# Performance work log

Measured on AMD Instinct MI355X. Metric: run time of the kernel, lower is better.

## Reference

```python
import jax, jax.numpy as jnp
import numpy as np

DIM = 1024
NUM_HEADS = 16
MASKED = True


def setup_inputs() -> dict:
    key = jax.random.key(0)
    ks = jax.random.split(key, 9)
    B, S, D = 2, 2048, DIM
    return {
        "x": jax.random.normal(ks[0], (B, S, D), dtype=jnp.float32),
        "Wq": jax.random.normal(ks[1], (D, D), dtype=jnp.float32),
        "bq": jax.random.normal(ks[2], (D,), dtype=jnp.float32),
        "Wk": jax.random.normal(ks[3], (D, D), dtype=jnp.float32),
        "bk": jax.random.normal(ks[4], (D,), dtype=jnp.float32),
        "Wv": jax.random.normal(ks[5], (D, D), dtype=jnp.float32),
        "bv": jax.random.normal(ks[6], (D,), dtype=jnp.float32),
        "Wo": jax.random.normal(ks[7], (D, D), dtype=jnp.float32),
        "bo": jax.random.normal(ks[8], (D,), dtype=jnp.float32),
    }


def _mha(x, Wq, bq, Wk, bk, Wv, bv, Wo, bo):
    B, S, D = x.shape
    H = NUM_HEADS
    hd = D // H
    # projections (torch Linear stores [out,in]; here W is [out,in], x @ W.T + b)
    q = x @ Wq.T + bq
    k = x @ Wk.T + bk
    v = x @ Wv.T + bv
    # [B, H, S, hd]
    q = q.reshape(B, S, H, hd).transpose(0, 2, 1, 3)
    k = k.reshape(B, S, H, hd).transpose(0, 2, 1, 3)
    v = v.reshape(B, S, H, hd).transpose(0, 2, 1, 3)
    scores = jnp.einsum("bhqd,bhkd->bhqk", q, k) / jnp.sqrt(jnp.asarray(hd, x.dtype))
    if MASKED:
        mask = jnp.tril(jnp.ones((S, S), dtype=bool))
        scores = jnp.where(mask, scores, -jnp.inf)
    attn = jax.nn.softmax(scores, axis=-1)
    out = jnp.einsum("bhqk,bhkd->bhqd", attn, v)
    out = out.transpose(0, 2, 1, 3).reshape(B, S, D)
    return out @ Wo.T + bo


def reference(x, Wq, bq, Wk, bk, Wv, bv, Wo, bo):
    return _mha(x, Wq, bq, Wk, bk, Wv, bv, Wo, bo)
```

## Files before the change

kernel.cpp:

```cpp
#include <hip/hip_runtime.h>

typedef unsigned short u16;
typedef unsigned int u32;
typedef __attribute__((ext_vector_type(4))) float f32x4;
typedef __attribute__((ext_vector_type(8))) __bf16 bf16x8;

#define L2E 1.4426950408889634f

__device__ __forceinline__ u16 f2bf(float f) { return __builtin_bit_cast(u16, (__bf16)f); }
__device__ __forceinline__ float bf2f(u16 h) { return (float)__builtin_bit_cast(__bf16, h); }
__device__ __forceinline__ f32x4 mfma16(bf16x8 a, bf16x8 b, f32x4 c) {
  return __builtin_amdgcn_mfma_f32_16x16x32_bf16(a, b, c, 0, 0, 0);
}
__device__ __forceinline__ void gl_lds16(const u16* g, u16* l) {
  __builtin_amdgcn_global_load_lds((__attribute__((address_space(1))) void*)g,
                                   (__attribute__((address_space(3))) void*)l,
                                   16, 0, 0);
}
__device__ __forceinline__ f32x4 fzero() {
  f32x4 v = {0.f, 0.f, 0.f, 0.f};
  return v;
}

__global__ void k_prep(const float* __restrict__ x, const float* __restrict__ Wq,
                       const float* __restrict__ Wk, const float* __restrict__ Wv,
                       const float* __restrict__ Wo,
                       u16* __restrict__ xh, u16* __restrict__ xl,
                       u16* __restrict__ wqh, u16* __restrict__ wql,
                       u16* __restrict__ wkh, u16* __restrict__ wkl,
                       u16* __restrict__ wvb, u16* __restrict__ wob) {
  int i = (blockIdx.x * 256 + threadIdx.x) * 4;
  const float* src;
  u16* hi;
  u16* lo;
  int j;
  if (i < 4194304)      { src = x;  hi = xh;  lo = xl;      j = i; }
  else if (i < 5242880) { src = Wq; hi = wqh; lo = wql;     j = i - 4194304; }
  else if (i < 6291456) { src = Wk; hi = wkh; lo = wkl;     j = i - 5242880; }
  else if (i < 7340032) { src = Wv; hi = wvb; lo = nullptr; j = i - 6291456; }
  else                  { src = Wo; hi = wob; lo = nullptr; j = i - 7340032; }
  float4 v = *(const float4*)(src + j);
  float vv[4] = {v.x, v.y, v.z, v.w};
  u16 hh[4];
#pragma unroll
  for (int t = 0; t < 4; ++t) hh[t] = f2bf(vv[t]);
  *(ushort4*)(hi + j) = make_ushort4(hh[0], hh[1], hh[2], hh[3]);
  if (lo) {
    u16 ll[4];
#pragma unroll
    for (int t = 0; t < 4; ++t) ll[t] = f2bf(vv[t] - bf2f(hh[t]));
    *(ushort4*)(lo + j) = make_ushort4(ll[0], ll[1], ll[2], ll[3]);
  }
}

template <int SPLIT, int EPI>
__device__ __forceinline__ void gemm_body(
    u16* sm, const u16* __restrict__ Ah, const u16* __restrict__ Al,
    const u16* __restrict__ Bh, const u16* __restrict__ Bl,
    const float* __restrict__ bias, float scale,
    u16* __restrict__ oH, u16* __restrict__ oL, float* __restrict__ oF,
    int m0, int n0) {
  u16* sAh = sm;
  u16* sBh = sm + 8192;
  u16* sAl = SPLIT ? (sm + 16384) : sm;
  u16* sBl = SPLIT ? (sm + 24576) : sm;

  const int tid = threadIdx.x;
  const int lane = tid & 63, w = tid >> 6;
  const int wm = w >> 1, wn = w & 1;
  const int fr = lane & 15, fg = lane >> 4;
  const int strow = tid >> 3;
  const int stcb = (tid & 7) * 16;

  f32x4 acc[4][4];
#pragma unroll
  for (int i = 0; i < 4; ++i)
#pragma unroll
    for (int j = 0; j < 4; ++j) acc[i][j] = fzero();

  for (int kk = 0; kk < 1024; kk += 64) {
    __syncthreads();
#pragma unroll
    for (int c = 0; c < 4; ++c) {
      int row = c * 32 + strow;
      int srcc = (stcb ^ (((row >> 2) & 1) << 5)) >> 1;
      int dstc = row * 64 + (stcb >> 1);
      gl_lds16(Ah + (size_t)(m0 + row) * 1024 + kk + srcc, sAh + dstc);
      gl_lds16(Bh + (size_t)(n0 + row) * 1024 + kk + srcc, sBh + dstc);
      if constexpr (SPLIT) {
        gl_lds16(Al + (size_t)(m0 + row) * 1024 + kk + srcc, sAl + dstc);
        gl_lds16(Bl + (size_t)(n0 + row) * 1024 + kk + srcc, sBl + dstc);
      }
    }
    __syncthreads();

#pragma unroll
    for (int kk2 = 0; kk2 < 2; ++kk2) {
      bf16x8 ah[4], bh[4], al[4], bl[4];
#pragma unroll
      for (int i = 0; i < 4; ++i) {
        int ra = wm * 64 + i * 16 + fr;
        int ca = (kk2 * 64 + fg * 16) ^ (((ra >> 2) & 1) << 5);
        ah[i] = *(const bf16x8*)(sAh + ra * 64 + (ca >> 1));
        if constexpr (SPLIT) al[i] = *(const bf16x8*)(sAl + ra * 64 + (ca >> 1));
        int rb = wn * 64 + i * 16 + fr;
        int cb = (kk2 * 64 + fg * 16) ^ (((rb >> 2) & 1) << 5);
        bh[i] = *(const bf16x8*)(sBh + rb * 64 + (cb >> 1));
        if constexpr (SPLIT) bl[i] = *(const bf16x8*)(sBl + rb * 64 + (cb >> 1));
      }
      __builtin_amdgcn_s_setprio(1);
#pragma unroll
      for (int i = 0; i < 4; ++i)
#pragma unroll
        for (int j = 0; j < 4; ++j) {
          acc[i][j] = mfma16(ah[i], bh[j], acc[i][j]);
          if constexpr (SPLIT) {
            acc[i][j] = mfma16(ah[i], bl[j], acc[i][j]);
            acc[i][j] = mfma16(al[i], bh[j], acc[i][j]);
          }
        }
      __builtin_amdgcn_s_setprio(0);
    }
  }

#pragma unroll
  for (int i = 0; i < 4; ++i)
#pragma unroll
    for (int j = 0; j < 4; ++j) {
      int cg = n0 + wn * 64 + j * 16 + fr;
      float bv = bias[cg];
      if constexpr (EPI == 1) {
        int rgb = m0 + wm * 64 + i * 16 + fg * 4;
        int b = rgb >> 11, s = rgb & 2047, hd2 = cg >> 6, dd = cg & 63;
        u16 hv[4];
#pragma unroll
        for (int r = 0; r < 4; ++r) hv[r] = f2bf((acc[i][j][r] + bv) * scale);
        *(ushort4*)(oH + ((size_t)((b * 16 + hd2) * 64 + dd)) * 2048 + s) =
            make_ushort4(hv[0], hv[1], hv[2], hv[3]);
      } else {
#pragma unroll
        for (int r = 0; r < 4; ++r) {
          int rg = m0 + wm * 64 + i * 16 + fg * 4 + r;
          float val = (acc[i][j][r] + bv) * scale;
          if constexpr (EPI == 0) {
            int b = rg >> 11, s = rg & 2047, hd2 = cg >> 6, dd = cg & 63;
            size_t off = ((size_t)((b * 16 + hd2) * 2048 + s)) * 64 + dd;
            u16 hv = f2bf(val);
            oH[off] = hv;
            oL[off] = f2bf(val - bf2f(hv));
          } else {
            oF[(size_t)rg * 1024 + cg] = val;
          }
        }
      }
    }
}

__global__ __launch_bounds__(256, 2) void k_qkv(
    const u16* __restrict__ xh, const u16* __restrict__ xl,
    const u16* __restrict__ wqh, const u16* __restrict__ wql,
    const u16* __restrict__ wkh, const u16* __restrict__ wkl,
    const u16* __restrict__ wvb,
    const float* __restrict__ bq, const float* __restrict__ bk,
    const float* __restrict__ bv,
    u16* __restrict__ qh, u16* __restrict__ ql,
    u16* __restrict__ kh, u16* __restrict__ kl, u16* __restrict__ vt) {
  __shared__ u16 sm[32768];
  const int d = blockIdx.x;
  const int xcd = d & 7, j = d >> 3;
  const int m0 = (xcd * 4 + (j & 3)) * 128;
  const int pn = j >> 2;
  const int proj = pn >> 3, n0 = (pn & 7) * 128;
  if (proj == 0)
    gemm_body<1, 0>(sm, xh, xl, wqh, wql, bq, 0.125f * L2E, qh, ql, nullptr, m0, n0);
  else if (proj == 1)
    gemm_body<1, 0>(sm, xh, xl, wkh, wkl, bk, 1.0f, kh, kl, nullptr, m0, n0);
  else
    gemm_body<0, 1>(sm, xh, nullptr, wvb, nullptr, bv, 1.0f, vt, nullptr, nullptr, m0, n0);
}

__global__ __launch_bounds__(256, 4) void k_oproj(
    const u16* __restrict__ A, const u16* __restrict__ B,
    const float* __restrict__ bias, float* __restrict__ out) {
  __shared__ u16 sm[12288];
  u16* sA = sm;
  u16* sB = sm + 4096;

  const int tid = threadIdx.x;
  const int lane = tid & 63, w = tid >> 6;
  const int fr = lane & 15, fg = lane >> 4;
  const int m0 = blockIdx.x * 64, n0 = blockIdx.y * 128;
  const int strow = tid >> 3;
  const int stcb = (tid & 7) * 16;

  f32x4 acc[4][2];
#pragma unroll
  for (int i = 0; i < 4; ++i)
#pragma unroll
    for (int jj = 0; jj < 2; ++jj) acc[i][jj] = fzero();

  for (int kk = 0; kk < 1024; kk += 64) {
    __syncthreads();
#pragma unroll
    for (int c = 0; c < 2; ++c) {
      int row = c * 32 + strow;
      int srcc = (stcb ^ (((row >> 2) & 1) << 5)) >> 1;
      gl_lds16(A + (size_t)(m0 + row) * 1024 + kk + srcc, sA + row * 64 + (stcb >> 1));
    }
#pragma unroll
    for (int c = 0; c < 4; ++c) {
      int row = c * 32 + strow;
      int srcc = (stcb ^ (((row >> 2) & 1) << 5)) >> 1;
      gl_lds16(B + (size_t)(n0 + row) * 1024 + kk + srcc, sB + row * 64 + (stcb >> 1));
    }
    __syncthreads();

#pragma unroll
    for (int kk2 = 0; kk2 < 2; ++kk2) {
      bf16x8 af[4], bf_[2];
#pragma unroll
      for (int i = 0; i < 4; ++i) {
        int ra = i * 16 + fr;
        int ca = (kk2 * 64 + fg * 16) ^ (((ra >> 2) & 1) << 5);
        af[i] = *(const bf16x8*)(sA + ra * 64 + (ca >> 1));
      }
#pragma unroll
      for (int jj = 0; jj < 2; ++jj) {
        int rb = w * 32 + jj * 16 + fr;
        int cb = (kk2 * 64 + fg * 16) ^ (((rb >> 2) & 1) << 5);
        bf_[jj] = *(const bf16x8*)(sB + rb * 64 + (cb >> 1));
      }
      __builtin_amdgcn_s_setprio(1);
#pragma unroll
      for (int i = 0; i < 4; ++i)
#pragma unroll
        for (int jj = 0; jj < 2; ++jj) acc[i][jj] = mfma16(af[i], bf_[jj], acc[i][jj]);
      __builtin_amdgcn_s_setprio(0);
    }
  }

#pragma unroll
  for (int i = 0; i < 4; ++i)
#pragma unroll
    for (int jj = 0; jj < 2; ++jj) {
      int cg = n0 + w * 32 + jj * 16 + fr;
      float bv = bias[cg];
#pragma unroll
      for (int r = 0; r < 4; ++r) {
        int rg = m0 + i * 16 + fg * 4 + r;
        out[(size_t)rg * 1024 + cg] = acc[i][jj][r] + bv;
      }
    }
}

__global__ __launch_bounds__(512, 2) void k_attn(
    const u16* __restrict__ Qh, const u16* __restrict__ Ql,
    const u16* __restrict__ Kh, const u16* __restrict__ Kl,
    const u16* __restrict__ Vt, u16* __restrict__ Oa) {
  __shared__ u16 sKh[3][4096], sKl[3][4096], sVt[3][4096];
  __shared__ u16 sP[8][1024];

  const int tid = threadIdx.x;
  const int lane = tid & 63, w = tid >> 6;
  const int fr = lane & 15, fg = lane >> 4;

  const int d = blockIdx.x;
  const int g = d >> 3;
  const int bh = (d & 7) * 4 + (g & 3);
  const int pr = g >> 2;

  const size_t base = (size_t)bh * 131072;
  const u16* Qh_p = Qh + base;
  const u16* Ql_p = Ql + base;
  const u16* Kh_p = Kh + base;
  const u16* Kl_p = Kl + base;
  const u16* Vt_p = Vt + base;
  const int bb = bh >> 4, hh = bh & 15;

  const int srow8 = tid >> 3, scb8 = tid & 7;

  auto STAGE = [&](int t, int c) {
    int cbs = scb8 ^ (srow8 & 7);
    gl_lds16(Kh_p + ((size_t)(t * 64 + srow8)) * 64 + cbs * 8, &sKh[c][srow8 * 64 + scb8 * 8]);
    gl_lds16(Kl_p + ((size_t)(t * 64 + srow8)) * 64 + cbs * 8, &sKl[c][srow8 * 64 + scb8 * 8]);
    gl_lds16(Vt_p + (size_t)srow8 * 2048 + t * 64 + cbs * 8, &sVt[c][srow8 * 64 + scb8 * 8]);
  };

  for (int half = 0; half < 2; ++half) {
    const int j = half ? (15 - pr) : pr;
    const int nt = 2 * (j + 1);
    const int qrow = j * 128 + w * 16 + fr;

    if (half) asm volatile("s_barrier" ::: "memory");
    int cur = 0;
    STAGE(0, 0);

    bf16x8 qhf[2], qlf[2];
#pragma unroll
    for (int ks = 0; ks < 2; ++ks) {
      qhf[ks] = *(const bf16x8*)(Qh_p + (size_t)qrow * 64 + ks * 32 + fg * 8);
      qlf[ks] = *(const bf16x8*)(Ql_p + (size_t)qrow * 64 + ks * 32 + fg * 8);
    }

    float mx = -1e30f, l = 0.f;
    f32x4 o[4];
#pragma unroll
    for (int f = 0; f < 4; ++f) o[f] = fzero();

    for (int t = 0; t < nt; ++t) {
      int nxt = cur + 1;
      if (nxt == 3) nxt = 0;
      if (t + 1 < nt) {
        STAGE(t + 1, nxt);
        asm volatile("s_waitcnt vmcnt(3)" ::: "memory");
      } else {
        asm volatile("s_waitcnt vmcnt(0)" ::: "memory");
      }
      asm volatile("s_barrier" ::: "memory");

      const u16* kbh = sKh[cur];
      const u16* kbl = sKl[cur];
      const u16* vbb = sVt[cur];

      f32x4 sc[4];
      __builtin_amdgcn_s_setprio(1);
#pragma unroll
      for (int f = 0; f < 4; ++f) {
        f32x4 a = fzero();
#pragma unroll
        for (int ks = 0; ks < 2; ++ks) {
          int row = f * 16 + fr;
          int cb = (fg + 4 * ks) ^ (fr & 7);
          bf16x8 khv = *(const bf16x8*)(kbh + row * 64 + cb * 8);
          bf16x8 klv = *(const bf16x8*)(kbl + row * 64 + cb * 8);
          a = mfma16(khv, qhf[ks], a);
          a = mfma16(khv, qlf[ks], a);
          a = mfma16(klv, qhf[ks], a);
        }
        sc[f] = a;
      }
      __builtin_amdgcn_s_setprio(0);

      if (t >= nt - 2) {
#pragma unroll
        for (int f = 0; f < 4; ++f)
#pragma unroll
          for (int r = 0; r < 4; ++r) {
            int kvg = t * 64 + f * 16 + fg * 4 + r;
            if (kvg > qrow) sc[f][r] = -1e30f;
          }
      }

      float pm = -1e30f;
#pragma unroll
      for (int f = 0; f < 4; ++f)
#pragma unroll
        for (int r = 0; r < 4; ++r) pm = fmaxf(pm, sc[f][r]);
      pm = fmaxf(pm, __shfl_xor(pm, 16, 64));
      pm = fmaxf(pm, __shfl_xor(pm, 32, 64));

      const bool resc = __any(pm > mx + 11.5f);
      float alp = 1.0f;
      if (resc) {
        float mn = fmaxf(mx, pm);
        alp = exp2f(mx - mn);
        mx = mn;
      }

      float ps = 0.f;
#pragma unroll
      for (int f = 0; f < 4; ++f) {
        float p0 = exp2f(sc[f][0] - mx);
        float p1 = exp2f(sc[f][1] - mx);
        float p2 = exp2f(sc[f][2] - mx);
        float p3 = exp2f(sc[f][3] - mx);
        ps += (p0 + p1) + (p2 + p3);
        uint2 pv;
        pv.x = (u32)f2bf(p0) | ((u32)f2bf(p1) << 16);
        pv.y = (u32)f2bf(p2) | ((u32)f2bf(p3) << 16);
        int e = (f * 16 + fg * 4) ^ ((fr & 7) << 3);
        *(uint2*)(&sP[w][fr * 64 + e]) = pv;
      }
      ps += __shfl_xor(ps, 16, 64);
      ps += __shfl_xor(ps, 32, 64);
      l = l * alp + ps;

      if (resc) {
        float alpb[4];
#pragma unroll
        for (int r = 0; r < 4; ++r) alpb[r] = __shfl(alp, fg * 4 + r, 64);
#pragma unroll
        for (int f = 0; f < 4; ++f)
#pragma unroll
          for (int r = 0; r < 4; ++r) o[f][r] *= alpb[r];
      }

      __builtin_amdgcn_s_setprio(1);
#pragma unroll
      for (int ks = 0; ks < 2; ++ks) {
        int e = (ks * 32 + fg * 8) ^ ((fr & 7) << 3);
        bf16x8 pa = *(const bf16x8*)(&sP[w][fr * 64 + e]);
#pragma unroll
        for (int f = 0; f < 4; ++f) {
          int row = f * 16 + fr;
          int cb = (fg + 4 * ks) ^ (fr & 7);
          bf16x8 vb = *(const bf16x8*)(vbb + row * 64 + cb * 8);
          o[f] = mfma16(pa, vb, o[f]);
        }
      }
      __builtin_amdgcn_s_setprio(0);

      cur = nxt;
    }

    float lb[4];
#pragma unroll
    for (int r = 0; r < 4; ++r) lb[r] = __shfl(l, fg * 4 + r, 64);
#pragma unroll
    for (int f = 0; f < 4; ++f)
#pragma unroll
      for (int r = 0; r < 4; ++r) {
        int qg = j * 128 + w * 16 + fg * 4 + r;
        float val = o[f][r] / lb[r];
        Oa[((size_t)(bb * 2048 + qg)) * 1024 + hh * 64 + f * 16 + fr] = f2bf(val);
      }
  }
}

extern "C" void kernel_launch(void* const* d_in, const int* in_sizes, int n_in,
                              void* d_out, int out_size, void* d_ws, size_t ws_size,
                              hipStream_t stream) {
  const float* x  = (const float*)d_in[0];
  const float* Wq = (const float*)d_in[1];
  const float* bq = (const float*)d_in[2];
  const float* Wk = (const float*)d_in[3];
  const float* bk = (const float*)d_in[4];
  const float* Wv = (const float*)d_in[5];
  const float* bv = (const float*)d_in[6];
  const float* Wo = (const float*)d_in[7];
  const float* bo = (const float*)d_in[8];
  float* out = (float*)d_out;

  u16* ws  = (u16*)d_ws;
  u16* xh  = ws;
  u16* xl  = xh + 4194304;
  u16* wqh = xl + 4194304;
  u16* wql = wqh + 1048576;
  u16* wkh = wql + 1048576;
  u16* wkl = wkh + 1048576;
  u16* wvb = wkl + 1048576;
  u16* wob = wvb + 1048576;
  u16* qh  = wob + 1048576;
  u16* ql  = qh + 4194304;
  u16* kh  = ql + 4194304;
  u16* kl  = kh + 4194304;
  u16* vt  = kl + 4194304;
  u16* ao  = xh;

  k_prep<<<8192, 256, 0, stream>>>(x, Wq, Wk, Wv, Wo, xh, xl, wqh, wql, wkh, wkl, wvb, wob);
  k_qkv<<<768, 256, 0, stream>>>(xh, xl, wqh, wql, wkh, wkl, wvb, bq, bk, bv,
                                 qh, ql, kh, kl, vt);
  k_attn<<<256, 512, 0, stream>>>(qh, ql, kh, kl, vt, ao);
  k_oproj<<<dim3(64, 8), 256, 0, stream>>>(ao, wob, bo, out);
}
```

Measured before the change: 154.7 us.

## Keep softmax probabilities in registers by permuting K rows, shrink attention blocks

Staging now permutes K rows in LDS so the score MFMA output layout lines up with the A-operand layout of the PV MFMA. Probabilities are then converted to bf16 in registers, which removes the per-wave sP LDS round trip. Blocks shrink from 512 to 256 threads, each covering 64 query rows, and the grid doubles to 512 with a reworked causal pairing. Each thread now issues twice as many staging loads, and K/V tiles are reused across fewer query rows.

```diff
diff --git a/kernel.cpp b/kernel.cpp
--- a/kernel.cpp
+++ b/kernel.cpp
@@ -253,12 +253,11 @@
     }
 }
 
-__global__ __launch_bounds__(512, 2) void k_attn(
+__global__ __launch_bounds__(256, 2) void k_attn(
     const u16* __restrict__ Qh, const u16* __restrict__ Ql,
     const u16* __restrict__ Kh, const u16* __restrict__ Kl,
     const u16* __restrict__ Vt, u16* __restrict__ Oa) {
   __shared__ u16 sKh[3][4096], sKl[3][4096], sVt[3][4096];
-  __shared__ u16 sP[8][1024];
 
   const int tid = threadIdx.x;
   const int lane = tid & 63, w = tid >> 6;
@@ -277,19 +276,24 @@
   const u16* Vt_p = Vt + base;
   const int bb = bh >> 4, hh = bh & 15;
 
-  const int srow8 = tid >> 3, scb8 = tid & 7;
+  const int srow = tid >> 3, scb8 = tid & 7;
 
   auto STAGE = [&](int t, int c) {
-    int cbs = scb8 ^ (srow8 & 7);
-    gl_lds16(Kh_p + ((size_t)(t * 64 + srow8)) * 64 + cbs * 8, &sKh[c][srow8 * 64 + scb8 * 8]);
-    gl_lds16(Kl_p + ((size_t)(t * 64 + srow8)) * 64 + cbs * 8, &sKl[c][srow8 * 64 + scb8 * 8]);
-    gl_lds16(Vt_p + (size_t)srow8 * 2048 + t * 64 + cbs * 8, &sVt[c][srow8 * 64 + scb8 * 8]);
+#pragma unroll
+    for (int r2 = 0; r2 < 2; ++r2) {
+      int prow = r2 * 32 + srow;
+      int kvs = (prow & 32) | ((prow & 16) >> 2) | ((prow & 12) << 1) | (prow & 3);
+      int cbk = scb8 ^ (prow & 7);
+      gl_lds16(Kh_p + ((size_t)(t * 64 + kvs)) * 64 + cbk * 8, &sKh[c][prow * 64 + scb8 * 8]);
+      gl_lds16(Kl_p + ((size_t)(t * 64 + kvs)) * 64 + cbk * 8, &sKl[c][prow * 64 + scb8 * 8]);
+      gl_lds16(Vt_p + (size_t)prow * 2048 + t * 64 + cbk * 8, &sVt[c][prow * 64 + scb8 * 8]);
+    }
   };
 
   for (int half = 0; half < 2; ++half) {
-    const int j = half ? (15 - pr) : pr;
-    const int nt = 2 * (j + 1);
-    const int qrow = j * 128 + w * 16 + fr;
+    const int j = half ? (31 - pr) : pr;
+    const int nt = j + 1;
+    const int qrow = j * 64 + w * 16 + fr;
 
     if (half) asm volatile("s_barrier" ::: "memory");
     int cur = 0;
@@ -312,7 +316,7 @@
       if (nxt == 3) nxt = 0;
       if (t + 1 < nt) {
         STAGE(t + 1, nxt);
-        asm volatile("s_waitcnt vmcnt(3)" ::: "memory");
+        asm volatile("s_waitcnt vmcnt(6)" ::: "memory");
       } else {
         asm volatile("s_waitcnt vmcnt(0)" ::: "memory");
       }
@@ -341,14 +345,14 @@
       }
       __builtin_amdgcn_s_setprio(0);
 
-      if (t >= nt - 2) {
-#pragma unroll
-        for (int f = 0; f < 4; ++f)
-#pragma unroll
-          for (int r = 0; r < 4; ++r) {
-            int kvg = t * 64 + f * 16 + fg * 4 + r;
-            if (kvg > qrow) sc[f][r] = -1e30f;
-          }
+      if (t == nt - 1) {
+#pragma unroll
+        for (int f = 0; f < 4; ++f) {
+          int kvb = t * 64 + (f >> 1) * 32 + fg * 8 + (f & 1) * 4;
+#pragma unroll
+          for (int r = 0; r < 4; ++r)
+            if (kvb + r > qrow) sc[f][r] = -1e30f;
+        }
       }
 
       float pm = -1e30f;
@@ -367,19 +371,15 @@
         mx = mn;
       }
 
+      float pp[4][4];
       float ps = 0.f;
 #pragma unroll
       for (int f = 0; f < 4; ++f) {
-        float p0 = exp2f(sc[f][0] - mx);
-        float p1 = exp2f(sc[f][1] - mx);
-        float p2 = exp2f(sc[f][2] - mx);
-        float p3 = exp2f(sc[f][3] - mx);
-        ps += (p0 + p1) + (p2 + p3);
-        uint2 pv;
-        pv.x = (u32)f2bf(p0) | ((u32)f2bf(p1) << 16);
-        pv.y = (u32)f2bf(p2) | ((u32)f2bf(p3) << 16);
-        int e = (f * 16 + fg * 4) ^ ((fr & 7) << 3);
-        *(uint2*)(&sP[w][fr * 64 + e]) = pv;
+#pragma unroll
+        for (int r = 0; r < 4; ++r) {
+          pp[f][r] = exp2f(sc[f][r] - mx);
+          ps += pp[f][r];
+        }
       }
       ps += __shfl_xor(ps, 16, 64);
       ps += __shfl_xor(ps, 32, 64);
@@ -398,8 +398,12 @@
       __builtin_amdgcn_s_setprio(1);
 #pragma unroll
       for (int ks = 0; ks < 2; ++ks) {
-        int e = (ks * 32 + fg * 8) ^ ((fr & 7) << 3);
-        bf16x8 pa = *(const bf16x8*)(&sP[w][fr * 64 + e]);
+        bf16x8 pa;
+#pragma unroll
+        for (int jj = 0; jj < 4; ++jj) {
+          pa[jj] = (__bf16)pp[2 * ks][jj];
+          pa[4 + jj] = (__bf16)pp[2 * ks + 1][jj];
+        }
 #pragma unroll
         for (int f = 0; f < 4; ++f) {
           int row = f * 16 + fr;
@@ -420,7 +424,7 @@
     for (int f = 0; f < 4; ++f)
 #pragma unroll
       for (int r = 0; r < 4; ++r) {
-        int qg = j * 128 + w * 16 + fg * 4 + r;
+        int qg = j * 64 + w * 16 + fg * 4 + r;
         float val = o[f][r] / lb[r];
         Oa[((size_t)(bb * 2048 + qg)) * 1024 + hh * 64 + f * 16 + fr] = f2bf(val);
       }
@@ -460,6 +464,6 @@
   k_prep<<<8192, 256, 0, stream>>>(x, Wq, Wk, Wv, Wo, xh, xl, wqh, wql, wkh, wkl, wvb, wob);
   k_qkv<<<768, 256, 0, stream>>>(xh, xl, wqh, wql, wkh, wkl, wvb, bq, bk, bv,
                                  qh, ql, kh, kl, vt);
-  k_attn<<<256, 512, 0, stream>>>(qh, ql, kh, kl, vt, ao);
+  k_attn<<<512, 256, 0, stream>>>(qh, ql, kh, kl, vt, ao);
   k_oproj<<<dim3(64, 8), 256, 0, stream>>>(ao, wob, bo, out);
 }
```

Measured after the change: 152.0 us. About the same (-1.8%).
